# Optimization experiments

Measured on AMD Instinct MI355X. Metric: run time of the kernel, lower is better.

The kernel has to match this reference:

```python
import jax, jax.numpy as jnp
import numpy as np

T_SCHEDULE = 999.0
LOG_2PI = float(np.log(2.0 * np.pi))


def setup_inputs() -> dict:
    key = jax.random.key(0)
    k1, k2, k3 = jax.random.split(key, 3)
    xt = jax.random.normal(k1, (128, 3, 32, 32), dtype=jnp.float32)
    # integer-style diffusion timesteps in [0, 900); divided by t_schedule=999 inside
    t = jax.random.uniform(k2, (128,), dtype=jnp.float32) * 900.0
    gt_images = jax.random.normal(k3, (20000, 3, 32, 32), dtype=jnp.float32)
    return {"xt": xt, "t": t, "gt_images": gt_images}


def reference(xt, t, gt_images):
    # AnalyticFlow.forward_fast
    B = xt.shape[0]
    N = gt_images.shape[0]
    x = jax.lax.stop_gradient(xt.reshape(B, -1))  # original detaches x
    gt = gt_images.reshape(N, -1)                 # [N, D]
    D = x.shape[-1]
    tt = t / T_SCHEDULE                           # [B]
    sig = 1.0 - tt                                # [B]
    # log N(term_2; 0, I) summed over D, where term_2 = (x - t*gt)/(1-t).
    # ||x - t*gt||^2 = ||x||^2 - 2 t x.gt + t^2 ||gt||^2  (avoids B*N*D tensor)
    x2 = jnp.sum(x * x, axis=-1)                  # [B]
    g2 = jnp.sum(gt * gt, axis=-1)                # [N]
    xg = x @ gt.T                                 # [B, N] GEMM
    sq = x2[:, None] - 2.0 * tt[:, None] * xg + (tt * tt)[:, None] * g2[None, :]
    log_p = -0.5 * sq / (sig * sig)[:, None] - 0.5 * D * LOG_2PI  # [B, N]
    log_p = log_p - jnp.max(log_p)                # global-max shift as in original
    eta = jax.nn.softmax(log_p, axis=1)           # [B, N], rows sum to 1
    # drift = mean_n (N*eta_n) * (gt_n - x)/(1-t) = (eta @ gt - x)/(1-t)
    drift = (eta @ gt - x) / sig[:, None]         # [B, D]
    return drift.reshape(xt.shape)
```

## Files before the change

### kernel.cpp

```cpp
#include <hip/hip_runtime.h>
#include <stdint.h>

#define B_SZ   128
#define D_SZ   3072
#define N_SZ   20000
#define NPAD   20480

typedef __attribute__((ext_vector_type(8))) short  short8;
typedef __attribute__((ext_vector_type(4))) float  f32x4;

__device__ __forceinline__ unsigned short f2bf(float f) {
    unsigned u = __float_as_uint(f);
    u += 0x7FFFu + ((u >> 16) & 1u);
    return (unsigned short)(u >> 16);
}
__device__ __forceinline__ float bf2f(unsigned short h) {
    return __uint_as_float(((unsigned)h) << 16);
}

__device__ __forceinline__ void gl_lds16(const void* g, void* l) {
    __builtin_amdgcn_global_load_lds(
        (const __attribute__((address_space(1))) void*)g,
        (__attribute__((address_space(3))) void*)l, 16, 0, 0);
}

__global__ __launch_bounds__(256) void prep_x(const float* __restrict__ x,
                                              unsigned short* __restrict__ xhi,
                                              unsigned short* __restrict__ xlo)
{
    int i = blockIdx.x * 256 + threadIdx.x;
    float v = x[i];
    unsigned short h = f2bf(v);
    xhi[i] = h;
    xlo[i] = f2bf(v - bf2f(h));
}

__global__ __launch_bounds__(256) void scores_kernel(
        const float* __restrict__ gt,
        const unsigned short* __restrict__ xhi,
        const unsigned short* __restrict__ xlo,
        const float* __restrict__ tarr,
        float* __restrict__ S)
{
    __shared__ __align__(16) unsigned short Xhi_t[128 * 32];
    __shared__ __align__(16) unsigned short Xlo_t[128 * 32];
    __shared__ __align__(16) unsigned short Ghi_t[64 * 32];
    __shared__ __align__(16) unsigned short Glo_t[64 * 32];
    __shared__ float c1buf[128];
    __shared__ float c2buf[128];
    __shared__ float g2buf[64];

    const int tid   = threadIdx.x;
    const int nbase = blockIdx.x * 64;

    if (tid < 128) {
        float tt  = tarr[tid] / 999.0f;
        float sig = 1.0f - tt;
        float inv = 1.0f / (sig * sig);
        c1buf[tid] = tt * inv;
        c2buf[tid] = 0.5f * tt * tt * inv;
    }

    const int lane = tid & 63;
    const int wave = tid >> 6;
    const int mh = wave & 1;
    const int nh = wave >> 1;
    const int lm = lane & 15;
    const int qd = lane >> 4;

    const int gn = tid >> 2;
    const int gq = tid & 3;
    int grow = nbase + gn;
    if (grow > N_SZ - 1) grow = N_SZ - 1;
    const float* gp0 = gt + (size_t)grow * D_SZ + gq * 8;

    float g2acc = 0.0f;

    f32x4 acc[4][2];
    #pragma unroll
    for (int i = 0; i < 4; i++)
        #pragma unroll
        for (int j = 0; j < 2; j++)
            acc[i][j] = (f32x4){0.f, 0.f, 0.f, 0.f};

    for (int k0 = 0; k0 < D_SZ; k0 += 32) {
        #pragma unroll
        for (int i = 0; i < 2; i++) {
            int o  = (i * 256 + tid) * 16;
            int r  = o >> 6;
            int ke = (o & 63) >> 1;
            gl_lds16(xhi + (size_t)r * D_SZ + k0 + ke, (char*)Xhi_t + o);
            gl_lds16(xlo + (size_t)r * D_SZ + k0 + ke, (char*)Xlo_t + o);
        }
        f32x4 v0 = *(const f32x4*)(gp0 + k0);
        f32x4 v1 = *(const f32x4*)(gp0 + k0 + 4);
        short8 h8, l8;
        #pragma unroll
        for (int j = 0; j < 4; j++) {
            float a = v0[j], b = v1[j];
            unsigned short ha = f2bf(a), hb = f2bf(b);
            h8[j]     = (short)ha;  h8[j + 4] = (short)hb;
            l8[j]     = (short)f2bf(a - bf2f(ha));
            l8[j + 4] = (short)f2bf(b - bf2f(hb));
            g2acc += a * a + b * b;
        }
        *(short8*)&Ghi_t[gn * 32 + gq * 8] = h8;
        *(short8*)&Glo_t[gn * 32 + gq * 8] = l8;

        __syncthreads();

        short8 bhi[2], blo[2];
        #pragma unroll
        for (int ni = 0; ni < 2; ni++) {
            int r = nh * 32 + ni * 16 + lm;
            bhi[ni] = *(short8*)&Ghi_t[r * 32 + qd * 8];
            blo[ni] = *(short8*)&Glo_t[r * 32 + qd * 8];
        }
        #pragma unroll
        for (int mi = 0; mi < 4; mi++) {
            int r = mh * 64 + mi * 16 + lm;
            short8 ahi = *(short8*)&Xhi_t[r * 32 + qd * 8];
            short8 alo = *(short8*)&Xlo_t[r * 32 + qd * 8];
            #pragma unroll
            for (int ni = 0; ni < 2; ni++) {
                acc[mi][ni] = __builtin_amdgcn_mfma_f32_16x16x32_bf16(ahi, bhi[ni], acc[mi][ni], 0, 0, 0);
                acc[mi][ni] = __builtin_amdgcn_mfma_f32_16x16x32_bf16(ahi, blo[ni], acc[mi][ni], 0, 0, 0);
                acc[mi][ni] = __builtin_amdgcn_mfma_f32_16x16x32_bf16(alo, bhi[ni], acc[mi][ni], 0, 0, 0);
            }
        }
        __syncthreads();
    }

    g2acc += __shfl_xor(g2acc, 1);
    g2acc += __shfl_xor(g2acc, 2);
    if (gq == 0) g2buf[gn] = g2acc;
    __syncthreads();

    #pragma unroll
    for (int mi = 0; mi < 4; mi++) {
        #pragma unroll
        for (int ni = 0; ni < 2; ni++) {
            int ncol = nh * 32 + ni * 16 + lm;
            int ng = nbase + ncol;
            if (ng < N_SZ) {
                float g2 = g2buf[ncol];
                #pragma unroll
                for (int i = 0; i < 4; i++) {
                    int m = mh * 64 + mi * 16 + qd * 4 + i;
                    S[(size_t)m * NPAD + ng] = c1buf[m] * acc[mi][ni][i] - c2buf[m] * g2;
                }
            }
        }
    }
}

__global__ __launch_bounds__(256) void softmax_stats(
        const float* __restrict__ S,
        unsigned short* __restrict__ P,
        float* __restrict__ L)
{
    const int b = blockIdx.x;
    const int tid = threadIdx.x;
    const int lane = tid & 63;
    const int wave = tid >> 6;
    const float* row = S + (size_t)b * NPAD;
    __shared__ float wred[4];

    float mx = -3.402823466e+38f;
    for (int n = tid; n < N_SZ; n += 256) mx = fmaxf(mx, row[n]);
    #pragma unroll
    for (int o = 32; o > 0; o >>= 1) mx = fmaxf(mx, __shfl_xor(mx, o));
    if (lane == 0) wred[wave] = mx;
    __syncthreads();
    mx = fmaxf(fmaxf(wred[0], wred[1]), fmaxf(wred[2], wred[3]));
    __syncthreads();

    float sum = 0.f;
    unsigned short* prow = P + (size_t)b * NPAD;
    for (int n = tid; n < NPAD; n += 256) {
        float p = 0.f;
        if (n < N_SZ) { p = expf(row[n] - mx); sum += p; }
        prow[n] = f2bf(p);
    }
    #pragma unroll
    for (int o = 32; o > 0; o >>= 1) sum += __shfl_xor(sum, o);
    if (lane == 0) wred[wave] = sum;
    __syncthreads();
    if (tid == 0) L[b] = wred[0] + wred[1] + wred[2] + wred[3];
}

__global__ __launch_bounds__(256) void zero_f32(float* __restrict__ p)
{
    p[blockIdx.x * 256 + threadIdx.x] = 0.f;
}

__global__ __launch_bounds__(256) void drift_kernel(
        const float* __restrict__ gt,
        const unsigned short* __restrict__ P,
        float* __restrict__ Dacc)
{
    __shared__ __align__(16) unsigned short Pt[128 * 32];
    __shared__ __align__(16) unsigned short Gt[128 * 40];

    const int tid = threadIdx.x;
    const int nt = blockIdx.x % 24;
    const int kc = blockIdx.x / 24;
    const int dbase = nt * 128;

    const int lane = tid & 63;
    const int wave = tid >> 6;
    const int mh = wave & 1;
    const int dh = wave >> 1;
    const int lm = lane & 15;
    const int qd = lane >> 4;

    const int dg = tid & 31;
    const int kq = tid >> 5;

    f32x4 acc[4][4];
    #pragma unroll
    for (int i = 0; i < 4; i++)
        #pragma unroll
        for (int j = 0; j < 4; j++)
            acc[i][j] = (f32x4){0.f, 0.f, 0.f, 0.f};

    for (int s = 0; s < 40; s++) {
        int kb = kc * 1280 + s * 32;
        #pragma unroll
        for (int i = 0; i < 2; i++) {
            int o  = (i * 256 + tid) * 16;
            int r  = o >> 6;
            int ke = (o & 63) >> 1;
            gl_lds16(P + (size_t)r * NPAD + kb + ke, (char*)Pt + o);
        }
        f32x4 row[4];
        #pragma unroll
        for (int i = 0; i < 4; i++) {
            int kg = kb + kq * 4 + i;
            if (kg > N_SZ - 1) kg = N_SZ - 1;
            row[i] = *(const f32x4*)(gt + (size_t)kg * D_SZ + dbase + dg * 4);
        }
        #pragma unroll
        for (int j = 0; j < 4; j++) {
            unsigned long long pk =
                  (unsigned long long)f2bf(row[0][j])
                | ((unsigned long long)f2bf(row[1][j]) << 16)
                | ((unsigned long long)f2bf(row[2][j]) << 32)
                | ((unsigned long long)f2bf(row[3][j]) << 48);
            *(unsigned long long*)((char*)Gt + (size_t)(dg * 4 + j) * 80 + kq * 8) = pk;
        }
        __syncthreads();

        short8 af[4], bf8[4];
        #pragma unroll
        for (int mi = 0; mi < 4; mi++)
            af[mi] = *(short8*)&Pt[(mh * 64 + mi * 16 + lm) * 32 + qd * 8];
        #pragma unroll
        for (int ni = 0; ni < 4; ni++)
            bf8[ni] = *(short8*)((char*)Gt + (size_t)(dh * 64 + ni * 16 + lm) * 80 + qd * 16);
        #pragma unroll
        for (int mi = 0; mi < 4; mi++)
            #pragma unroll
            for (int ni = 0; ni < 4; ni++)
                acc[mi][ni] = __builtin_amdgcn_mfma_f32_16x16x32_bf16(af[mi], bf8[ni], acc[mi][ni], 0, 0, 0);
        __syncthreads();
    }

    #pragma unroll
    for (int mi = 0; mi < 4; mi++)
        #pragma unroll
        for (int ni = 0; ni < 4; ni++) {
            int d = dbase + dh * 64 + ni * 16 + lm;
            #pragma unroll
            for (int i = 0; i < 4; i++) {
                int m = mh * 64 + mi * 16 + qd * 4 + i;
                atomicAdd(&Dacc[(size_t)m * D_SZ + d], acc[mi][ni][i]);
            }
        }
}

__global__ __launch_bounds__(256) void epilogue_kernel(
        const float* __restrict__ Dacc, const float* __restrict__ L,
        const float* __restrict__ x, const float* __restrict__ tarr,
        float* __restrict__ out)
{
    int i = blockIdx.x * 256 + threadIdx.x;
    int b = i / D_SZ;
    float tt = tarr[b] / 999.0f;
    float sig = 1.0f - tt;
    out[i] = (Dacc[i] / L[b] - x[i]) / sig;
}

extern "C" void kernel_launch(void* const* d_in, const int* in_sizes, int n_in,
                              void* d_out, int out_size, void* d_ws, size_t ws_size,
                              hipStream_t stream)
{
    const float* xt = (const float*)d_in[0];
    const float* t  = (const float*)d_in[1];
    const float* gt = (const float*)d_in[2];
    float* out = (float*)d_out;

    char* ws = (char*)d_ws;
    unsigned short* Xhi = (unsigned short*)(ws + 0);
    unsigned short* Xlo = (unsigned short*)(ws + 786432);
    float*          S   = (float*)         (ws + 1572864);
    unsigned short* P   = (unsigned short*)(ws + 12058624);
    float*          L   = (float*)         (ws + 17301504);
    float*          Dacc= (float*)         (ws + 17302528);

    prep_x        <<<1536, 256, 0, stream>>>(xt, Xhi, Xlo);
    scores_kernel <<< 313, 256, 0, stream>>>(gt, Xhi, Xlo, t, S);
    softmax_stats <<< 128, 256, 0, stream>>>(S, P, L);
    zero_f32      <<<1536, 256, 0, stream>>>(Dacc);
    drift_kernel  <<< 384, 256, 0, stream>>>(gt, P, Dacc);
    epilogue_kernel<<<1536, 256, 0, stream>>>(Dacc, L, xt, t, out);
}
```

Measured before the change: 522.3 us.

## Split-K scores and drift GEMMs with atomics; parallelize softmax across row chunks

The scores GEMM becomes split-K over 8 chunks of D, with 2504 blocks instead of 313, accumulating x·gt and ||gt||^2 through float atomics into zeroed buffers. The softmax is split into a max kernel that uses an order-preserving key atomicMax and an exp/sum kernel, each running 8 blocks per row, and the score constants are applied on the fly. The drift GEMM's split-K grows from 16 to 40 chunks (960 blocks). The aim is to fill the GPU's CUs, which the earlier grids left underused. The cost is many global atomics, a larger zeroing pass, and nondeterministic summation order.

```diff
diff --git a/kernel.cpp b/kernel.cpp
--- a/kernel.cpp
+++ b/kernel.cpp
@@ -17,11 +17,23 @@
 __device__ __forceinline__ float bf2f(unsigned short h) {
     return __uint_as_float(((unsigned)h) << 16);
 }
+__device__ __forceinline__ unsigned fkey_enc(float f) {
+    unsigned b = __float_as_uint(f);
+    return (b & 0x80000000u) ? ~b : (b | 0x80000000u);
+}
+__device__ __forceinline__ float fkey_dec(unsigned u) {
+    return __uint_as_float((u & 0x80000000u) ? (u ^ 0x80000000u) : ~u);
+}
 
 __device__ __forceinline__ void gl_lds16(const void* g, void* l) {
     __builtin_amdgcn_global_load_lds(
         (const __attribute__((address_space(1))) void*)g,
         (__attribute__((address_space(3))) void*)l, 16, 0, 0);
+}
+
+__global__ __launch_bounds__(256) void zero_ws(float* __restrict__ p)
+{
+    p[blockIdx.x * 256 + threadIdx.x] = 0.f;
 }
 
 __global__ __launch_bounds__(256) void prep_x(const float* __restrict__ x,
@@ -39,27 +51,19 @@
         const float* __restrict__ gt,
         const unsigned short* __restrict__ xhi,
         const unsigned short* __restrict__ xlo,
-        const float* __restrict__ tarr,
-        float* __restrict__ S)
+        float* __restrict__ XG,
+        float* __restrict__ G2)
 {
     __shared__ __align__(16) unsigned short Xhi_t[128 * 32];
     __shared__ __align__(16) unsigned short Xlo_t[128 * 32];
     __shared__ __align__(16) unsigned short Ghi_t[64 * 32];
     __shared__ __align__(16) unsigned short Glo_t[64 * 32];
-    __shared__ float c1buf[128];
-    __shared__ float c2buf[128];
-    __shared__ float g2buf[64];
 
     const int tid   = threadIdx.x;
-    const int nbase = blockIdx.x * 64;
-
-    if (tid < 128) {
-        float tt  = tarr[tid] / 999.0f;
-        float sig = 1.0f - tt;
-        float inv = 1.0f / (sig * sig);
-        c1buf[tid] = tt * inv;
-        c2buf[tid] = 0.5f * tt * tt * inv;
-    }
+    const int kc    = blockIdx.x & 7;
+    const int nt    = blockIdx.x >> 3;
+    const int nbase = nt * 64;
+    const int kcb   = kc * 384;
 
     const int lane = tid & 63;
     const int wave = tid >> 6;
@@ -70,9 +74,9 @@
 
     const int gn = tid >> 2;
     const int gq = tid & 3;
-    int grow = nbase + gn;
-    if (grow > N_SZ - 1) grow = N_SZ - 1;
-    const float* gp0 = gt + (size_t)grow * D_SZ + gq * 8;
+    const int ng0 = nbase + gn;
+    int grow = ng0 > N_SZ - 1 ? N_SZ - 1 : ng0;
+    const float* gp0 = gt + (size_t)grow * D_SZ + kcb + gq * 8;
 
     float g2acc = 0.0f;
 
@@ -83,14 +87,14 @@
         for (int j = 0; j < 2; j++)
             acc[i][j] = (f32x4){0.f, 0.f, 0.f, 0.f};
 
-    for (int k0 = 0; k0 < D_SZ; k0 += 32) {
+    for (int k0 = 0; k0 < 384; k0 += 32) {
         #pragma unroll
         for (int i = 0; i < 2; i++) {
             int o  = (i * 256 + tid) * 16;
             int r  = o >> 6;
             int ke = (o & 63) >> 1;
-            gl_lds16(xhi + (size_t)r * D_SZ + k0 + ke, (char*)Xhi_t + o);
-            gl_lds16(xlo + (size_t)r * D_SZ + k0 + ke, (char*)Xlo_t + o);
+            gl_lds16(xhi + (size_t)r * D_SZ + kcb + k0 + ke, (char*)Xhi_t + o);
+            gl_lds16(xlo + (size_t)r * D_SZ + kcb + k0 + ke, (char*)Xlo_t + o);
         }
         f32x4 v0 = *(const f32x4*)(gp0 + k0);
         f32x4 v1 = *(const f32x4*)(gp0 + k0 + 4);
@@ -133,8 +137,7 @@
 
     g2acc += __shfl_xor(g2acc, 1);
     g2acc += __shfl_xor(g2acc, 2);
-    if (gq == 0) g2buf[gn] = g2acc;
-    __syncthreads();
+    if (gq == 0 && ng0 < N_SZ) atomicAdd(&G2[ng0], g2acc);
 
     #pragma unroll
     for (int mi = 0; mi < 4; mi++) {
@@ -143,55 +146,73 @@
             int ncol = nh * 32 + ni * 16 + lm;
             int ng = nbase + ncol;
             if (ng < N_SZ) {
-                float g2 = g2buf[ncol];
                 #pragma unroll
                 for (int i = 0; i < 4; i++) {
                     int m = mh * 64 + mi * 16 + qd * 4 + i;
-                    S[(size_t)m * NPAD + ng] = c1buf[m] * acc[mi][ni][i] - c2buf[m] * g2;
+                    atomicAdd(&XG[(size_t)m * NPAD + ng], acc[mi][ni][i]);
                 }
             }
         }
     }
 }
 
-__global__ __launch_bounds__(256) void softmax_stats(
-        const float* __restrict__ S,
-        unsigned short* __restrict__ P,
-        float* __restrict__ L)
-{
-    const int b = blockIdx.x;
+__global__ __launch_bounds__(256) void maxk(
+        const float* __restrict__ XG, const float* __restrict__ G2,
+        const float* __restrict__ tarr, unsigned* __restrict__ Mkey)
+{
+    const int b  = blockIdx.x >> 3;
+    const int ch = blockIdx.x & 7;
     const int tid = threadIdx.x;
-    const int lane = tid & 63;
-    const int wave = tid >> 6;
-    const float* row = S + (size_t)b * NPAD;
+    float tt  = tarr[b] / 999.0f;
+    float sig = 1.0f - tt;
+    float inv = 1.0f / (sig * sig);
+    float c1 = tt * inv, c2 = 0.5f * tt * tt * inv;
+    const float* xg = XG + (size_t)b * NPAD;
     __shared__ float wred[4];
 
     float mx = -3.402823466e+38f;
-    for (int n = tid; n < N_SZ; n += 256) mx = fmaxf(mx, row[n]);
+    int n0 = ch * 2560;
+    for (int n = n0 + tid; n < n0 + 2560; n += 256)
+        if (n < N_SZ) mx = fmaxf(mx, c1 * xg[n] - c2 * G2[n]);
     #pragma unroll
     for (int o = 32; o > 0; o >>= 1) mx = fmaxf(mx, __shfl_xor(mx, o));
-    if (lane == 0) wred[wave] = mx;
+    if ((tid & 63) == 0) wred[tid >> 6] = mx;
     __syncthreads();
-    mx = fmaxf(fmaxf(wred[0], wred[1]), fmaxf(wred[2], wred[3]));
+    if (tid == 0) {
+        mx = fmaxf(fmaxf(wred[0], wred[1]), fmaxf(wred[2], wred[3]));
+        atomicMax(&Mkey[b], fkey_enc(mx));
+    }
+}
+
+__global__ __launch_bounds__(256) void expk(
+        const float* __restrict__ XG, const float* __restrict__ G2,
+        const float* __restrict__ tarr, const unsigned* __restrict__ Mkey,
+        unsigned short* __restrict__ P, float* __restrict__ L)
+{
+    const int b  = blockIdx.x >> 3;
+    const int ch = blockIdx.x & 7;
+    const int tid = threadIdx.x;
+    float tt  = tarr[b] / 999.0f;
+    float sig = 1.0f - tt;
+    float inv = 1.0f / (sig * sig);
+    float c1 = tt * inv, c2 = 0.5f * tt * tt * inv;
+    float m = fkey_dec(Mkey[b]);
+    const float* xg = XG + (size_t)b * NPAD;
+    unsigned short* prow = P + (size_t)b * NPAD;
+    __shared__ float wred[4];
+
+    float sum = 0.f;
+    int n0 = ch * 2560;
+    for (int n = n0 + tid; n < n0 + 2560; n += 256) {
+        float p = 0.f;
+        if (n < N_SZ) { p = expf(c1 * xg[n] - c2 * G2[n] - m); sum += p; }
+        prow[n] = f2bf(p);
+    }
+    #pragma unroll
+    for (int o = 32; o > 0; o >>= 1) sum += __shfl_xor(sum, o);
+    if ((tid & 63) == 0) wred[tid >> 6] = sum;
     __syncthreads();
-
-    float sum = 0.f;
-    unsigned short* prow = P + (size_t)b * NPAD;
-    for (int n = tid; n < NPAD; n += 256) {
-        float p = 0.f;
-        if (n < N_SZ) { p = expf(row[n] - mx); sum += p; }
-        prow[n] = f2bf(p);
-    }
-    #pragma unroll
-    for (int o = 32; o > 0; o >>= 1) sum += __shfl_xor(sum, o);
-    if (lane == 0) wred[wave] = sum;
-    __syncthreads();
-    if (tid == 0) L[b] = wred[0] + wred[1] + wred[2] + wred[3];
-}
-
-__global__ __launch_bounds__(256) void zero_f32(float* __restrict__ p)
-{
-    p[blockIdx.x * 256 + threadIdx.x] = 0.f;
+    if (tid == 0) atomicAdd(&L[b], wred[0] + wred[1] + wred[2] + wred[3]);
 }
 
 __global__ __launch_bounds__(256) void drift_kernel(
@@ -224,8 +245,8 @@
         for (int j = 0; j < 4; j++)
             acc[i][j] = (f32x4){0.f, 0.f, 0.f, 0.f};
 
-    for (int s = 0; s < 40; s++) {
-        int kb = kc * 1280 + s * 32;
+    for (int s = 0; s < 16; s++) {
+        int kb = kc * 512 + s * 32;
         #pragma unroll
         for (int i = 0; i < 2; i++) {
             int o  = (i * 256 + tid) * 16;
@@ -301,17 +322,20 @@
     float* out = (float*)d_out;
 
     char* ws = (char*)d_ws;
-    unsigned short* Xhi = (unsigned short*)(ws + 0);
-    unsigned short* Xlo = (unsigned short*)(ws + 786432);
-    float*          S   = (float*)         (ws + 1572864);
-    unsigned short* P   = (unsigned short*)(ws + 12058624);
-    float*          L   = (float*)         (ws + 17301504);
-    float*          Dacc= (float*)         (ws + 17302528);
-
-    prep_x        <<<1536, 256, 0, stream>>>(xt, Xhi, Xlo);
-    scores_kernel <<< 313, 256, 0, stream>>>(gt, Xhi, Xlo, t, S);
-    softmax_stats <<< 128, 256, 0, stream>>>(S, P, L);
-    zero_f32      <<<1536, 256, 0, stream>>>(Dacc);
-    drift_kernel  <<< 384, 256, 0, stream>>>(gt, P, Dacc);
+    float*          XG  = (float*)         (ws + 0);
+    float*          G2  = (float*)         (ws + 10485760);
+    float*          Dacc= (float*)         (ws + 10567680);
+    unsigned*       Mkey= (unsigned*)      (ws + 12140544);
+    float*          L   = (float*)         (ws + 12141056);
+    unsigned short* Xhi = (unsigned short*)(ws + 12141568);
+    unsigned short* Xlo = (unsigned short*)(ws + 12928000);
+    unsigned short* P   = (unsigned short*)(ws + 13714432);
+
+    zero_ws       <<<11857, 256, 0, stream>>>((float*)ws);
+    prep_x        <<< 1536, 256, 0, stream>>>(xt, Xhi, Xlo);
+    scores_kernel <<< 2504, 256, 0, stream>>>(gt, Xhi, Xlo, XG, G2);
+    maxk          <<< 1024, 256, 0, stream>>>(XG, G2, t, Mkey);
+    expk          <<< 1024, 256, 0, stream>>>(XG, G2, t, Mkey, P, L);
+    drift_kernel  <<<  960, 256, 0, stream>>>(gt, P, Dacc);
     epilogue_kernel<<<1536, 256, 0, stream>>>(Dacc, L, xt, t, out);
 }
```

Measured after the change: 494.1 us. 1.06x faster.
